# Kernel tuning notes

Measured on AMD Instinct MI355X. Metric: run time of the kernel, lower is better.

## Reference

```python
import jax, jax.numpy as jnp
import numpy as np

B, C, M, T = 2, 512, 16, 128
H = 8
D = C // H  # 64, divisible by 4 for 2D RoPE
G = C // 4  # GroupNorm groups = 128
S = M * T


def group_norm(x, scale, bias, groups=G, eps=1e-5):
    b, c, m, t = x.shape
    xg = x.reshape(b, groups, c // groups, m, t)
    mu = xg.mean(axis=(2, 3, 4), keepdims=True)
    var = xg.var(axis=(2, 3, 4), keepdims=True)
    xn = ((xg - mu) * jax.lax.rsqrt(var + eps)).reshape(b, c, m, t)
    return xn * scale[None, :, None, None] + bias[None, :, None, None]


def dwsep_conv(x, dw, pw):
    # depthwise 3x3 (groups=C) then pointwise 1x1
    y = jax.lax.conv_general_dilated(
        x, dw, window_strides=(1, 1), padding='SAME',
        dimension_numbers=('NCHW', 'HWIO', 'NCHW'), feature_group_count=x.shape[1])
    return jnp.einsum('bcmt,cd->bdmt', y, pw)


def rope2d(x):
    # x: [B,H,M,T,D]; first D/2 dims rotated by freq index m, last D/2 by time index t
    d = x.shape[-1]
    dh = d // 2
    q = dh // 2
    inv = 1.0 / (10000.0 ** (jnp.arange(q, dtype=jnp.float32) / q))

    def rot(v, ang):
        h = v.shape[-1] // 2
        v1, v2 = v[..., :h], v[..., h:]
        c, s = jnp.cos(ang), jnp.sin(ang)
        return jnp.concatenate([v1 * c - v2 * s, v1 * s + v2 * c], axis=-1)

    ang_f = jnp.arange(x.shape[2], dtype=jnp.float32)[:, None] * inv  # [M,q]
    ang_t = jnp.arange(x.shape[3], dtype=jnp.float32)[:, None] * inv  # [T,q]
    xf = rot(x[..., :dh], ang_f[:, None, :])  # broadcast over T
    xt = rot(x[..., dh:], ang_t)
    return jnp.concatenate([xf, xt], axis=-1)


def setup_inputs() -> dict:
    key = jax.random.key(0)
    ks = jax.random.split(key, 14)
    s = 0.02
    return {
        'x': jax.random.normal(ks[0], (B, C, M, T), jnp.float32),
        'lengths': jax.random.randint(ks[1], (B,), T // 2, T + 1),
        'gn_scale': jnp.ones((C,), jnp.float32),
        'gn_bias': jnp.zeros((C,), jnp.float32),
        'dw_q': jax.random.normal(ks[2], (3, 3, 1, C), jnp.float32) * s,
        'dw_k': jax.random.normal(ks[3], (3, 3, 1, C), jnp.float32) * s,
        'dw_v': jax.random.normal(ks[4], (3, 3, 1, C), jnp.float32) * s,
        'pw_q': jax.random.normal(ks[5], (C, C), jnp.float32) * s,
        'pw_k': jax.random.normal(ks[6], (C, C), jnp.float32) * s,
        'pw_v': jax.random.normal(ks[7], (C, C), jnp.float32) * s,
        'attn_w': jax.random.normal(ks[8], (C, C), jnp.float32) * s,
        'attn_b': jnp.zeros((C,), jnp.float32),
        'out_w': jax.random.normal(ks[9], (C, C), jnp.float32) * s,
        'out_b': jnp.zeros((C,), jnp.float32),
    }


def reference(x, lengths, gn_scale, gn_bias, dw_q, dw_k, dw_v, pw_q, pw_k, pw_v,
              attn_w, attn_b, out_w, out_b):
    residual = x
    xn = group_norm(x, gn_scale, gn_bias)

    def to_heads(y):  # [B,C,M,T] -> [B,H,M,T,D]
        return y.reshape(B, H, D, M, T).transpose(0, 1, 3, 4, 2)

    q = rope2d(to_heads(dwsep_conv(xn, dw_q, pw_q)))
    k = rope2d(to_heads(dwsep_conv(xn, dw_k, pw_k)))
    v = to_heads(dwsep_conv(xn, dw_v, pw_v))

    q = q.reshape(B, H, S, D)
    k = k.reshape(B, H, S, D)
    v = v.reshape(B, H, S, D)

    scores = jnp.einsum('bhsd,bhkd->bhsk', q, k) / np.sqrt(D).astype(np.float32)
    valid_t = jnp.arange(T)[None, :] < lengths[:, None]        # [B,T]
    valid = jnp.tile(valid_t, (1, M))                          # [B,S], token idx = m*T + t
    scores = jnp.where(valid[:, None, None, :], scores, jnp.float32(-1e9))
    attn = jax.nn.softmax(scores, axis=-1)
    o = jnp.einsum('bhsk,bhkd->bhsd', attn, v)                 # [B,H,S,D]

    o = o.transpose(0, 2, 1, 3).reshape(B, S, C)
    o = o @ attn_w + attn_b                                    # block output proj
    o = o.reshape(B, M, T, C).transpose(0, 3, 1, 2)            # [B,C,M,T]
    out = jnp.einsum('bcmt,cd->bdmt', o, out_w) + out_b[None, :, None, None]
    return residual + out
```

## Files before the change

### kernel.cpp

```cpp
#include <hip/hip_runtime.h>
#include <math.h>

#define CCH 512
#define SSQ 2048
#define MTOT 4096

typedef __bf16 bf16;
typedef __bf16 bf16x8 __attribute__((ext_vector_type(8)));
typedef __bf16 bf16x4 __attribute__((ext_vector_type(4)));
typedef float  f32x4  __attribute__((ext_vector_type(4)));

#define AS1 __attribute__((address_space(1)))
#define AS3 __attribute__((address_space(3)))
__device__ __forceinline__ void glds16(const void* g, void* l) {
    __builtin_amdgcn_global_load_lds((const AS1 void*)g, (AS3 void*)l, 16, 0, 0);
}

__global__ __launch_bounds__(256) void gnw_kernel(const float* __restrict__ x,
        float* __restrict__ mu, float* __restrict__ rstd,
        const float* __restrict__ w0, const float* __restrict__ w1,
        const float* __restrict__ w2, const float* __restrict__ w3,
        const float* __restrict__ w4, bf16* __restrict__ wT,
        const float* __restrict__ attnb, const float* __restrict__ outb,
        float* __restrict__ bcv) {
    __shared__ float smem[64*65];
    int tid = threadIdx.x;
    if (blockIdx.x < 256) {
        float* s_sum = smem;
        float* s_sq  = smem + 256;
        int bg = blockIdx.x;
        long base = (long)bg * 8192;
        float sum = 0.f, sq = 0.f;
#pragma unroll
        for (int r = 0; r < 32; ++r) {
            float v = x[base + r*256 + tid];
            sum += v; sq += v*v;
        }
        s_sum[tid] = sum; s_sq[tid] = sq;
        __syncthreads();
        for (int off = 128; off > 0; off >>= 1) {
            if (tid < off) { s_sum[tid] += s_sum[tid+off]; s_sq[tid] += s_sq[tid+off]; }
            __syncthreads();
        }
        if (tid == 0) {
            float m = s_sum[0] * (1.f/8192.f);
            float v = s_sq[0]  * (1.f/8192.f) - m*m;
            mu[bg] = m;
            rstd[bg] = rsqrtf(v + 1e-5f);
        }
    } else if (blockIdx.x < 576) {
        int bid = blockIdx.x - 256;
        int z = bid >> 6, r2 = bid & 63;
        int k0 = (r2 >> 3)*64, n0 = (r2 & 7)*64;
        const float* srcs[5] = {w0, w1, w2, w3, w4};
        const float* W = srcs[z];
        bf16* D = wT + (long)z * (CCH*CCH);
        float (*t)[65] = (float(*)[65])smem;
        int cI = tid & 63, r4 = tid >> 6;
#pragma unroll
        for (int p = 0; p < 16; ++p) {
            int kr = p*4 + r4;
            t[kr][cI] = W[(long)(k0+kr)*CCH + n0 + cI];
        }
        __syncthreads();
#pragma unroll
        for (int p = 0; p < 16; ++p) {
            int nr = p*4 + r4;
            D[(long)(n0+nr)*CCH + k0 + cI] = (bf16)t[cI][nr];
        }
    } else if (blockIdx.x < 578) {
        int n = (blockIdx.x - 576)*256 + tid;
        float a = outb[n];
#pragma unroll 16
        for (int j = 0; j < 512; ++j)
            a = fmaf(attnb[j], w4[(long)j*CCH + n], a);
        bcv[n] = a;
    } else {
        bf16* wAc = wT + (long)5*CCH*CCH;
        int base = (blockIdx.x - 578)*4096 + tid;
#pragma unroll
        for (int p = 0; p < 16; ++p)
            wAc[base + p*256] = (bf16)w3[base + p*256];
    }
}

__global__ void tn_kernel(const float* __restrict__ x, const float* __restrict__ mu,
                          const float* __restrict__ rstd, const float* __restrict__ gsc,
                          const float* __restrict__ gbs, bf16* __restrict__ xnT) {
    __shared__ float t[64][65];
    int s0 = blockIdx.x*64, c0 = blockIdx.y*64, b = blockIdx.z;
    int tid = threadIdx.x;
    int cI = tid & 63, r4 = tid >> 6;
#pragma unroll
    for (int p = 0; p < 16; ++p) {
        int cr = p*4 + r4;
        t[cr][cI] = x[((long)(b*CCH + c0 + cr))*SSQ + s0 + cI];
    }
    __syncthreads();
#pragma unroll
    for (int p = 0; p < 16; ++p) {
        int sr = p*4 + r4;
        int c = c0 + cI;
        int g = b*128 + (c >> 2);
        float v = (t[cI][sr] - mu[g]) * rstd[g] * gsc[c] + gbs[c];
        xnT[((long)(b*SSQ + s0 + sr))*CCH + c] = (bf16)v;
    }
}

__global__ __launch_bounds__(256) void dw3_kernel(const bf16* __restrict__ xnT,
        const float* __restrict__ dwq, const float* __restrict__ dwk,
        const float* __restrict__ dwv,
        bf16* __restrict__ yq, bf16* __restrict__ yk, bf16* __restrict__ yv) {
    int tid = threadIdx.x;
    int cc = (tid & 63) * 8;
    int s  = blockIdx.x*4 + (tid >> 6);
    int sl = s & (SSQ-1);
    int b  = s >> 11;
    int m = sl >> 7, t = sl & 127;
    float aq[8] = {}, ak[8] = {}, av[8] = {};
#pragma unroll
    for (int di = 0; di < 3; ++di) {
        int m2 = m + di - 1;
        if ((unsigned)m2 >= 16u) continue;
#pragma unroll
        for (int dj = 0; dj < 3; ++dj) {
            int t2 = t + dj - 1;
            if ((unsigned)t2 >= 128u) continue;
            bf16x8 xv = *(const bf16x8*)(xnT + ((long)(b*SSQ + m2*128 + t2))*CCH + cc);
            int wi = (di*3 + dj)*CCH + cc;
#pragma unroll
            for (int i = 0; i < 8; ++i) {
                float xf = (float)xv[i];
                aq[i] += xf * dwq[wi+i];
                ak[i] += xf * dwk[wi+i];
                av[i] += xf * dwv[wi+i];
            }
        }
    }
    bf16x8 oq, ok, ov;
#pragma unroll
    for (int i = 0; i < 8; ++i) { oq[i] = (bf16)aq[i]; ok[i] = (bf16)ak[i]; ov[i] = (bf16)av[i]; }
    long o = (long)s*CCH + cc;
    *(bf16x8*)(yq + o) = oq;
    *(bf16x8*)(yk + o) = ok;
    *(bf16x8*)(yv + o) = ov;
}

template<int NFR>
__device__ __forceinline__ void gemm_core128(const bf16* __restrict__ A,
        const bf16* __restrict__ Wt, int m0, int n0,
        bf16* As, bf16* Bs, f32x4 (&acc)[4][NFR]) {
    int tid = threadIdx.x, lane = tid & 63, wid = tid >> 6;
    int sw = wid & 1, nw = wid >> 1;
    int col = lane & 15, quad = lane >> 4;
    const char* gA[4]; char* ldsA[4];
#pragma unroll
    for (int p = 0; p < 4; ++p) {
        int ci = tid + p*256;
        int row = ci >> 3;
        int c = (ci & 7) ^ (row & 7);
        gA[p] = (const char*)A + ((long)(m0+row)*CCH + c*8)*2;
        ldsA[p] = (char*)As + ci*16;
    }
    const char* gB[NFR]; char* ldsB[NFR];
#pragma unroll
    for (int p = 0; p < NFR; ++p) {
        int ci = tid + p*256;
        int row = ci >> 3;
        int c = (ci & 7) ^ (row & 7);
        gB[p] = (const char*)Wt + ((long)(n0+row)*CCH + c*8)*2;
        ldsB[p] = (char*)Bs + ci*16;
    }
    int rowA = sw*64 + col;
    int rowB = nw*(NFR*16) + col;
    for (int k0 = 0; k0 < CCH; k0 += 64) {
        __syncthreads();
#pragma unroll
        for (int p = 0; p < 4; ++p)   glds16(gA[p] + k0*2, ldsA[p]);
#pragma unroll
        for (int p = 0; p < NFR; ++p) glds16(gB[p] + k0*2, ldsB[p]);
        __syncthreads();
        bf16x8 af[4][2], bfr[NFR][2];
#pragma unroll
        for (int mt = 0; mt < 4; ++mt) {
            int r = rowA + mt*16;
#pragma unroll
            for (int ks = 0; ks < 2; ++ks) {
                int c = (ks*4 + quad) ^ (r & 7);
                af[mt][ks] = *(const bf16x8*)((char*)As + r*128 + c*16);
            }
        }
#pragma unroll
        for (int nt = 0; nt < NFR; ++nt) {
            int r = rowB + nt*16;
#pragma unroll
            for (int ks = 0; ks < 2; ++ks) {
                int c = (ks*4 + quad) ^ (r & 7);
                bfr[nt][ks] = *(const bf16x8*)((char*)Bs + r*128 + c*16);
            }
        }
#pragma unroll
        for (int ks = 0; ks < 2; ++ks)
#pragma unroll
            for (int mt = 0; mt < 4; ++mt)
#pragma unroll
                for (int nt = 0; nt < NFR; ++nt)
                    acc[mt][nt] = __builtin_amdgcn_mfma_f32_16x16x32_bf16(
                        af[mt][ks], bfr[nt][ks], acc[mt][nt], 0,0,0);
    }
}

__global__ __launch_bounds__(256) void gemm_qkv(const bf16* __restrict__ Abase,
        bf16* __restrict__ wT, bf16* __restrict__ qout,
        bf16* __restrict__ kout, bf16* __restrict__ vout) {
    __shared__ bf16 As[128*64];
    __shared__ bf16 Bs[64*64];
    int z = blockIdx.z;
    if (z == 3 && blockIdx.x >= 4) return;
    int m0 = blockIdx.x*128, n0 = blockIdx.y*64;
    const bf16* Aop = (z < 3) ? Abase + (long)z*MTOT*CCH : wT + (long)4*CCH*CCH;
    const bf16* Wop = (z < 3) ? wT + (long)z*CCH*CCH   : wT + (long)5*CCH*CCH;
    f32x4 acc[4][2] = {};
    gemm_core128<2>(Aop, Wop, m0, n0, As, Bs, acc);
    int tid = threadIdx.x, lane = tid & 63, wid = tid >> 6;
    int sw = wid & 1, nw = wid >> 1;
    int col = lane & 15, quad = lane >> 4;
    int nb = n0 + nw*32, mb = m0 + sw*64;
    if (z == 3) {
        bf16* wCt = wT + (long)6*CCH*CCH;
#pragma unroll
        for (int nt = 0; nt < 2; ++nt) {
            int n = nb + nt*16 + col;
#pragma unroll
            for (int mt = 0; mt < 4; ++mt)
#pragma unroll
                for (int r = 0; r < 4; ++r)
                    wCt[(long)(mb + mt*16 + quad*4 + r)*CCH + n] = (bf16)acc[mt][nt][r];
        }
    } else if (z < 2) {
        bf16* outp = z ? kout : qout;
        const float sc = z ? 1.0f : 0.125f;
        float invf = __expf(-(float)col * 0.5756462732485114f);
        bool tHalf = (nb & 32) != 0;
#pragma unroll
        for (int mt = 0; mt < 4; ++mt)
#pragma unroll
            for (int r = 0; r < 4; ++r) {
                int row = mb + mt*16 + quad*4 + r;
                int sl = row & (SSQ-1);
                float pos = tHalf ? (float)(sl & 127) : (float)(sl >> 7);
                float ang = pos * invf;
                float sn, cs;
                __sincosf(ang, &sn, &cs);
                float x1 = acc[mt][0][r], x2 = acc[mt][1][r];
                outp[(long)row*CCH + nb + col]      = (bf16)((x1*cs - x2*sn)*sc);
                outp[(long)row*CCH + nb + 16 + col] = (bf16)((x1*sn + x2*cs)*sc);
            }
    } else {
#pragma unroll
        for (int mt = 0; mt < 4; ++mt)
#pragma unroll
            for (int nt = 0; nt < 2; ++nt) {
                int n = nb + nt*16 + col;
                int row0 = mb + mt*16 + quad*4;
                int bq = row0 >> 11, sl0 = row0 & (SSQ-1);
                bf16x4 pk;
#pragma unroll
                for (int r = 0; r < 4; ++r) pk[r] = (bf16)acc[mt][nt][r];
                *(bf16x4*)(vout + ((long)(bq*CCH + n))*SSQ + sl0) = pk;
            }
    }
}

__global__ __launch_bounds__(256) void gemm_out(const bf16* __restrict__ A,
        const bf16* __restrict__ Wt, const float* __restrict__ bias,
        const float* __restrict__ resid, float* __restrict__ outp) {
    __shared__ bf16 As[128*64];
    __shared__ bf16 Bs[64*64];
    int m0 = blockIdx.x*128, n0 = blockIdx.y*64;
    f32x4 acc[4][2] = {};
    gemm_core128<2>(A, Wt, m0, n0, As, Bs, acc);
    int tid = threadIdx.x, lane = tid & 63, wid = tid >> 6;
    int sw = wid & 1, nw = wid >> 1;
    int col = lane & 15, quad = lane >> 4;
    int nb = n0 + nw*32, mb = m0 + sw*64;
#pragma unroll
    for (int mt = 0; mt < 4; ++mt)
#pragma unroll
        for (int nt = 0; nt < 2; ++nt) {
            int n = nb + nt*16 + col;
            float bv = bias[n];
            int row0 = mb + mt*16 + quad*4;
            int b = row0 >> 11, sl0 = row0 & (SSQ-1);
            long off = ((long)(b*CCH + n))*SSQ + sl0;
            float4 rr = *(const float4*)(resid + off);
            float4 o4;
            o4.x = acc[mt][nt][0] + bv + rr.x;
            o4.y = acc[mt][nt][1] + bv + rr.y;
            o4.z = acc[mt][nt][2] + bv + rr.z;
            o4.w = acc[mt][nt][3] + bv + rr.w;
            *(float4*)(outp + off) = o4;
        }
}

__global__ __launch_bounds__(512, 4) void attn_kernel(
        const bf16* __restrict__ qb, const bf16* __restrict__ kb,
        const bf16* __restrict__ vb, const int* __restrict__ lengths,
        bf16* __restrict__ o) {
    __shared__ char KVs[2][32768];
    __shared__ float Lm[4][2][16];
    int bid = blockIdx.x;
    int bh = bid & 15, qtb = bid >> 4;
    int b = bh >> 3, h = bh & 7;
    int tid = threadIdx.x, wid = tid >> 6, lane = tid & 63;
    int col = lane & 15, quad = lane >> 4;
    int qh = wid & 3, kh = wid >> 2;
    int q0 = qtb*128 + qh*32;
    int thr = lengths[b] - 64 - quad*4;

    const char* gp[4]; int ldsoff[4];
#pragma unroll
    for (int p = 0; p < 4; ++p) {
        int idx = tid + p*512;
        int half = p >> 1;
        int rem = idx & 511;
        int r = rem >> 3;
        int csrc = (rem & 7) ^ (r & 7);
        if ((p & 1) == 0)
            gp[p] = (const char*)kb + ((long)(b*SSQ + half*1024 + r))*1024 + h*128 + csrc*16;
        else
            gp[p] = (const char*)vb + ((long)(b*CCH + h*64 + r))*4096 + half*2048 + csrc*16;
        ldsoff[p] = idx*16;
    }

    const bf16* qp = qb + (long)(b*SSQ)*CCH + h*64;
    bf16x8 qf[2][2];
#pragma unroll
    for (int qt2 = 0; qt2 < 2; ++qt2)
#pragma unroll
        for (int dc = 0; dc < 2; ++dc)
            qf[qt2][dc] = *(const bf16x8*)(qp + (long)(q0 + qt2*16 + col)*CCH + dc*32 + quad*8);

    f32x4 of[2][4] = {};
    float ls0 = 0.f, ls1 = 0.f;
    int cswz = col & 7;
    int kbase0 = col*128 + ((0*4 + quad) ^ cswz)*16;
    int kbase1 = col*128 + ((1*4 + quad) ^ cswz)*16;
    int qh2 = quad >> 1, qlo = (quad & 1)*8;
    int vlo0 = col*128 + ((0 + qh2) ^ cswz)*16 + qlo;
    int vhi0 = col*128 + ((4 + qh2) ^ cswz)*16 + qlo;
    int vlo1 = col*128 + ((2 + qh2) ^ cswz)*16 + qlo;
    int vhi1 = col*128 + ((6 + qh2) ^ cswz)*16 + qlo;

#pragma unroll
    for (int p = 0; p < 4; ++p) glds16(gp[p], KVs[0] + ldsoff[p]);
    __syncthreads();

    for (int t = 0; t < 16; ++t) {
        if (t < 15) {
#pragma unroll
            for (int p = 0; p < 4; ++p) {
                long step = (p & 1) ? 128L : 65536L;
                glds16(gp[p] + (long)(t+1)*step, KVs[(t+1) & 1] + ldsoff[p]);
            }
        }
        const char* K = KVs[t & 1] + kh*16384;
        const char* V = K + 8192;
        f32x4 sc[4][2];
        if (t & 1) {
#pragma unroll
            for (int sub = 0; sub < 4; ++sub) {
                f32x4 m;
#pragma unroll
                for (int r = 0; r < 4; ++r) m[r] = (sub*16 + r < thr) ? 0.f : -10000.f;
                sc[sub][0] = m; sc[sub][1] = m;
            }
        } else {
#pragma unroll
            for (int sub = 0; sub < 4; ++sub) {
                sc[sub][0] = (f32x4){0.f,0.f,0.f,0.f};
                sc[sub][1] = (f32x4){0.f,0.f,0.f,0.f};
            }
        }
        __builtin_amdgcn_s_setprio(1);
#pragma unroll
        for (int sub = 0; sub < 4; ++sub) {
            bf16x8 kf0 = *(const bf16x8*)(K + sub*2048 + kbase0);
            bf16x8 kf1 = *(const bf16x8*)(K + sub*2048 + kbase1);
            sc[sub][0] = __builtin_amdgcn_mfma_f32_16x16x32_bf16(kf0, qf[0][0], sc[sub][0], 0,0,0);
            sc[sub][1] = __builtin_amdgcn_mfma_f32_16x16x32_bf16(kf0, qf[1][0], sc[sub][1], 0,0,0);
            sc[sub][0] = __builtin_amdgcn_mfma_f32_16x16x32_bf16(kf1, qf[0][1], sc[sub][0], 0,0,0);
            sc[sub][1] = __builtin_amdgcn_mfma_f32_16x16x32_bf16(kf1, qf[1][1], sc[sub][1], 0,0,0);
        }
        __builtin_amdgcn_s_setprio(0);
#pragma unroll
        for (int ks = 0; ks < 2; ++ks) {
            bf16x8 pf[2];
#pragma unroll
            for (int qt2 = 0; qt2 < 2; ++qt2) {
                float s = 0.f;
#pragma unroll
                for (int r = 0; r < 4; ++r) {
                    float e0 = __expf(sc[ks][qt2][r]);
                    float e1 = __expf(sc[ks+2][qt2][r]);
                    pf[qt2][r]     = (bf16)e0;
                    pf[qt2][4 + r] = (bf16)e1;
                    s += e0 + e1;
                }
                if (qt2) ls1 += s; else ls0 += s;
            }
            int vlo = ks ? vlo1 : vlo0;
            int vhi = ks ? vhi1 : vhi0;
            __builtin_amdgcn_s_setprio(1);
#pragma unroll
            for (int dt = 0; dt < 4; ++dt) {
                bf16x4 lo = *(const bf16x4*)(V + dt*2048 + vlo);
                bf16x4 hi = *(const bf16x4*)(V + dt*2048 + vhi);
                bf16x8 vf = {lo[0],lo[1],lo[2],lo[3],hi[0],hi[1],hi[2],hi[3]};
                of[0][dt] = __builtin_amdgcn_mfma_f32_16x16x32_bf16(pf[0], vf, of[0][dt], 0,0,0);
                of[1][dt] = __builtin_amdgcn_mfma_f32_16x16x32_bf16(pf[1], vf, of[1][dt], 0,0,0);
            }
            __builtin_amdgcn_s_setprio(0);
        }
        __syncthreads();
    }

    ls0 += __shfl_xor(ls0, 16); ls0 += __shfl_xor(ls0, 32);
    ls1 += __shfl_xor(ls1, 16); ls1 += __shfl_xor(ls1, 32);

    float* Om = (float*)KVs;
    if (kh == 1) {
#pragma unroll
        for (int qt2 = 0; qt2 < 2; ++qt2)
#pragma unroll
            for (int dt = 0; dt < 4; ++dt)
#pragma unroll
                for (int r = 0; r < 4; ++r)
                    Om[(qh*32 + qt2*16 + quad*4 + r)*64 + dt*16 + col] = of[qt2][dt][r];
        if (quad == 0) { Lm[qh][0][col] = ls0; Lm[qh][1][col] = ls1; }
    }
    __syncthreads();
    if (kh == 0) {
        float i0 = 1.f / (ls0 + Lm[qh][0][col]);
        float i1 = 1.f / (ls1 + Lm[qh][1][col]);
        bf16* ob = o + (long)(b*SSQ + q0)*CCH + h*64;
#pragma unroll
        for (int qt2 = 0; qt2 < 2; ++qt2) {
            float inv = qt2 ? i1 : i0;
            float ir[4];
#pragma unroll
            for (int r = 0; r < 4; ++r) ir[r] = __shfl(inv, quad*4 + r);
#pragma unroll
            for (int dt = 0; dt < 4; ++dt)
#pragma unroll
                for (int r = 0; r < 4; ++r) {
                    float v = of[qt2][dt][r] + Om[(qh*32 + qt2*16 + quad*4 + r)*64 + dt*16 + col];
                    ob[(long)(qt2*16 + quad*4 + r)*CCH + dt*16 + col] = (bf16)(v * ir[r]);
                }
        }
    }
}

extern "C" void kernel_launch(void* const* d_in, const int* in_sizes, int n_in,
                              void* d_out, int out_size, void* d_ws, size_t ws_size,
                              hipStream_t stream) {
    const float* x        = (const float*)d_in[0];
    const int*   lengths  = (const int*)  d_in[1];
    const float* gn_scale = (const float*)d_in[2];
    const float* gn_bias  = (const float*)d_in[3];
    const float* dw_q     = (const float*)d_in[4];
    const float* dw_k     = (const float*)d_in[5];
    const float* dw_v     = (const float*)d_in[6];
    const float* pw_q     = (const float*)d_in[7];
    const float* pw_k     = (const float*)d_in[8];
    const float* pw_v     = (const float*)d_in[9];
    const float* attn_w   = (const float*)d_in[10];
    const float* attn_b   = (const float*)d_in[11];
    const float* out_w    = (const float*)d_in[12];
    const float* out_b    = (const float*)d_in[13];
    float* out = (float*)d_out;

    char* w = (char*)d_ws;
    float* mu   = (float*)w;
    float* rstd = (float*)(w + 1024);
    float* bcv  = (float*)(w + 2048);
    bf16* wT    = (bf16*)(w + 4096);
    bf16* wCt = wT + (long)6*CCH*CCH;
    bf16* xnT  = (bf16*)(w + 0x00400000);
    bf16* yT   = (bf16*)(w + 0x00800000);
    bf16* qbf  = (bf16*)(w + 0x01400000);
    bf16* kbf  = (bf16*)(w + 0x01800000);
    bf16* vbf  = (bf16*)(w + 0x01C00000);
    bf16* obf  = (bf16*)(w + 0x02000000);

    gnw_kernel<<<642, 256, 0, stream>>>(x, mu, rstd, pw_q, pw_k, pw_v, attn_w, out_w,
                                        wT, attn_b, out_b, bcv);
    tn_kernel<<<dim3(32,8,2), 256, 0, stream>>>(x, mu, rstd, gn_scale, gn_bias, xnT);
    dw3_kernel<<<MTOT/4, 256, 0, stream>>>(xnT, dw_q, dw_k, dw_v,
                                           yT, yT + (long)MTOT*CCH, yT + (long)2*MTOT*CCH);

    gemm_qkv<<<dim3(MTOT/128, CCH/64, 4), 256, 0, stream>>>(yT, wT, qbf, kbf, vbf);

    attn_kernel<<<256, 512, 0, stream>>>(qbf, kbf, vbf, lengths, obf);

    gemm_out<<<dim3(MTOT/128, CCH/64), 256, 0, stream>>>(obf, wCt, bcv, x, out);
}
```

Before: 176.9 us.

## Restructure attention to split keys across waves with 64-query blocks

The attention kernel now uses 256-thread blocks over 64 queries each (512 blocks). Each of the four waves handles a 32-key slice of every 128-key tile for all 64 queries, and the four partial outputs are reduced through LDS at the end. The V producer in the QKV GEMM writes a permuted sequence order so each lane can read V fragments with a single 16-byte LDS load instead of two 8-byte loads. The aim is more K/V fragment reuse across query tiles and fewer LDS reads, at the cost of a larger cross-wave reduction, more registers per wave and lower occupancy.

```diff
diff --git a/kernel.cpp b/kernel.cpp
--- a/kernel.cpp
+++ b/kernel.cpp
@@ -264,10 +264,12 @@
                 int n = nb + nt*16 + col;
                 int row0 = mb + mt*16 + quad*4;
                 int bq = row0 >> 11, sl0 = row0 & (SSQ-1);
+                int sub16 = (sl0 >> 4) & 1;
+                long slp = (long)(sl0 & ~31) + quad*8 + sub16*4;
                 bf16x4 pk;
 #pragma unroll
                 for (int r = 0; r < 4; ++r) pk[r] = (bf16)acc[mt][nt][r];
-                *(bf16x4*)(vout + ((long)(bq*CCH + n))*SSQ + sl0) = pk;
+                *(bf16x4*)(vout + ((long)(bq*CCH + n))*SSQ + slp) = pk;
             }
     }
 }
@@ -303,161 +305,139 @@
         }
 }
 
-__global__ __launch_bounds__(512, 4) void attn_kernel(
+__global__ __launch_bounds__(256, 2) void attn_kernel(
         const bf16* __restrict__ qb, const bf16* __restrict__ kb,
         const bf16* __restrict__ vb, const int* __restrict__ lengths,
         bf16* __restrict__ o) {
     __shared__ char KVs[2][32768];
-    __shared__ float Lm[4][2][16];
+    __shared__ float Lsm[4][4][16];
     int bid = blockIdx.x;
     int bh = bid & 15, qtb = bid >> 4;
     int b = bh >> 3, h = bh & 7;
     int tid = threadIdx.x, wid = tid >> 6, lane = tid & 63;
     int col = lane & 15, quad = lane >> 4;
-    int qh = wid & 3, kh = wid >> 2;
-    int q0 = qtb*128 + qh*32;
-    int thr = lengths[b] - 64 - quad*4;
-
-    const char* gp[4]; int ldsoff[4];
-#pragma unroll
-    for (int p = 0; p < 4; ++p) {
-        int idx = tid + p*512;
-        int half = p >> 1;
-        int rem = idx & 511;
-        int r = rem >> 3;
-        int csrc = (rem & 7) ^ (r & 7);
-        if ((p & 1) == 0)
-            gp[p] = (const char*)kb + ((long)(b*SSQ + half*1024 + r))*1024 + h*128 + csrc*16;
-        else
-            gp[p] = (const char*)vb + ((long)(b*CCH + h*64 + r))*4096 + half*2048 + csrc*16;
+    int q0 = qtb*64;
+    int lenb = lengths[b];
+    int thr = lenb - wid*32 - quad*4;
+
+    const char* gp[8]; int ldsoff[8];
+#pragma unroll
+    for (int p = 0; p < 8; ++p) {
+        int idx = p*256 + tid;
+        if (p < 4) {
+            int r = idx >> 3;
+            int csrc = (idx & 7) ^ (r & 7);
+            gp[p] = (const char*)kb + ((long)(b*SSQ + r))*1024 + h*128 + csrc*16;
+        } else {
+            int rem = idx & 1023;
+            int r = rem >> 4;
+            int csrc = (rem & 15) ^ (r & 15);
+            gp[p] = (const char*)vb + ((long)(b*CCH + h*64 + r))*4096 + csrc*16;
+        }
         ldsoff[p] = idx*16;
     }
 
     const bf16* qp = qb + (long)(b*SSQ)*CCH + h*64;
-    bf16x8 qf[2][2];
-#pragma unroll
-    for (int qt2 = 0; qt2 < 2; ++qt2)
+    bf16x8 qf[4][2];
+#pragma unroll
+    for (int qt = 0; qt < 4; ++qt)
 #pragma unroll
         for (int dc = 0; dc < 2; ++dc)
-            qf[qt2][dc] = *(const bf16x8*)(qp + (long)(q0 + qt2*16 + col)*CCH + dc*32 + quad*8);
-
-    f32x4 of[2][4] = {};
-    float ls0 = 0.f, ls1 = 0.f;
-    int cswz = col & 7;
-    int kbase0 = col*128 + ((0*4 + quad) ^ cswz)*16;
-    int kbase1 = col*128 + ((1*4 + quad) ^ cswz)*16;
-    int qh2 = quad >> 1, qlo = (quad & 1)*8;
-    int vlo0 = col*128 + ((0 + qh2) ^ cswz)*16 + qlo;
-    int vhi0 = col*128 + ((4 + qh2) ^ cswz)*16 + qlo;
-    int vlo1 = col*128 + ((2 + qh2) ^ cswz)*16 + qlo;
-    int vhi1 = col*128 + ((6 + qh2) ^ cswz)*16 + qlo;
-
-#pragma unroll
-    for (int p = 0; p < 4; ++p) glds16(gp[p], KVs[0] + ldsoff[p]);
+            qf[qt][dc] = *(const bf16x8*)(qp + (long)(q0 + qt*16 + col)*CCH + dc*32 + quad*8);
+
+    f32x4 of[4][4] = {};
+    float ls[4] = {};
+    int cswz7 = col & 7;
+    int kc0 = (quad ^ cswz7)*16;
+    int kc1 = ((4 + quad) ^ cswz7)*16;
+    int vaddr = col*256 + (((wid*4 + quad) ^ col) & 15)*16;
+
+#pragma unroll
+    for (int p = 0; p < 8; ++p) glds16(gp[p], KVs[0] + ldsoff[p]);
     __syncthreads();
 
     for (int t = 0; t < 16; ++t) {
         if (t < 15) {
 #pragma unroll
-            for (int p = 0; p < 4; ++p) {
-                long step = (p & 1) ? 128L : 65536L;
+            for (int p = 0; p < 8; ++p) {
+                const long step = (p < 4) ? 131072L : 256L;
                 glds16(gp[p] + (long)(t+1)*step, KVs[(t+1) & 1] + ldsoff[p]);
             }
         }
-        const char* K = KVs[t & 1] + kh*16384;
-        const char* V = K + 8192;
-        f32x4 sc[4][2];
-        if (t & 1) {
-#pragma unroll
-            for (int sub = 0; sub < 4; ++sub) {
-                f32x4 m;
-#pragma unroll
-                for (int r = 0; r < 4; ++r) m[r] = (sub*16 + r < thr) ? 0.f : -10000.f;
-                sc[sub][0] = m; sc[sub][1] = m;
-            }
-        } else {
-#pragma unroll
-            for (int sub = 0; sub < 4; ++sub) {
-                sc[sub][0] = (f32x4){0.f,0.f,0.f,0.f};
-                sc[sub][1] = (f32x4){0.f,0.f,0.f,0.f};
-            }
+        const char* K = KVs[t & 1] + wid*4096;
+        const char* V = KVs[t & 1] + 16384;
+        f32x4 sc[2][4];
+#pragma unroll
+        for (int sub = 0; sub < 2; ++sub) {
+            f32x4 m;
+#pragma unroll
+            for (int r = 0; r < 4; ++r) m[r] = (sub*16 + r < thr) ? 0.f : -10000.f;
+#pragma unroll
+            for (int qt = 0; qt < 4; ++qt) sc[sub][qt] = m;
         }
         __builtin_amdgcn_s_setprio(1);
 #pragma unroll
-        for (int sub = 0; sub < 4; ++sub) {
-            bf16x8 kf0 = *(const bf16x8*)(K + sub*2048 + kbase0);
-            bf16x8 kf1 = *(const bf16x8*)(K + sub*2048 + kbase1);
-            sc[sub][0] = __builtin_amdgcn_mfma_f32_16x16x32_bf16(kf0, qf[0][0], sc[sub][0], 0,0,0);
-            sc[sub][1] = __builtin_amdgcn_mfma_f32_16x16x32_bf16(kf0, qf[1][0], sc[sub][1], 0,0,0);
-            sc[sub][0] = __builtin_amdgcn_mfma_f32_16x16x32_bf16(kf1, qf[0][1], sc[sub][0], 0,0,0);
-            sc[sub][1] = __builtin_amdgcn_mfma_f32_16x16x32_bf16(kf1, qf[1][1], sc[sub][1], 0,0,0);
+        for (int sub = 0; sub < 2; ++sub) {
+            bf16x8 kf0 = *(const bf16x8*)(K + sub*2048 + col*128 + kc0);
+            bf16x8 kf1 = *(const bf16x8*)(K + sub*2048 + col*128 + kc1);
+#pragma unroll
+            for (int qt = 0; qt < 4; ++qt) {
+                sc[sub][qt] = __builtin_amdgcn_mfma_f32_16x16x32_bf16(kf0, qf[qt][0], sc[sub][qt], 0,0,0);
+                sc[sub][qt] = __builtin_amdgcn_mfma_f32_16x16x32_bf16(kf1, qf[qt][1], sc[sub][qt], 0,0,0);
+            }
         }
         __builtin_amdgcn_s_setprio(0);
-#pragma unroll
-        for (int ks = 0; ks < 2; ++ks) {
-            bf16x8 pf[2];
-#pragma unroll
-            for (int qt2 = 0; qt2 < 2; ++qt2) {
-                float s = 0.f;
-#pragma unroll
-                for (int r = 0; r < 4; ++r) {
-                    float e0 = __expf(sc[ks][qt2][r]);
-                    float e1 = __expf(sc[ks+2][qt2][r]);
-                    pf[qt2][r]     = (bf16)e0;
-                    pf[qt2][4 + r] = (bf16)e1;
-                    s += e0 + e1;
-                }
-                if (qt2) ls1 += s; else ls0 += s;
-            }
-            int vlo = ks ? vlo1 : vlo0;
-            int vhi = ks ? vhi1 : vhi0;
-            __builtin_amdgcn_s_setprio(1);
-#pragma unroll
-            for (int dt = 0; dt < 4; ++dt) {
-                bf16x4 lo = *(const bf16x4*)(V + dt*2048 + vlo);
-                bf16x4 hi = *(const bf16x4*)(V + dt*2048 + vhi);
-                bf16x8 vf = {lo[0],lo[1],lo[2],lo[3],hi[0],hi[1],hi[2],hi[3]};
-                of[0][dt] = __builtin_amdgcn_mfma_f32_16x16x32_bf16(pf[0], vf, of[0][dt], 0,0,0);
-                of[1][dt] = __builtin_amdgcn_mfma_f32_16x16x32_bf16(pf[1], vf, of[1][dt], 0,0,0);
-            }
-            __builtin_amdgcn_s_setprio(0);
-        }
+        bf16x8 pf[4];
+#pragma unroll
+        for (int qt = 0; qt < 4; ++qt) {
+            float s = 0.f;
+#pragma unroll
+            for (int r = 0; r < 4; ++r) {
+                float e0 = __expf(sc[0][qt][r]);
+                float e1 = __expf(sc[1][qt][r]);
+                pf[qt][r]     = (bf16)e0;
+                pf[qt][4 + r] = (bf16)e1;
+                s += e0 + e1;
+            }
+            ls[qt] += s;
+        }
+        __builtin_amdgcn_s_setprio(1);
+#pragma unroll
+        for (int dt = 0; dt < 4; ++dt) {
+            bf16x8 vf = *(const bf16x8*)(V + dt*4096 + vaddr);
+#pragma unroll
+            for (int qt = 0; qt < 4; ++qt)
+                of[qt][dt] = __builtin_amdgcn_mfma_f32_16x16x32_bf16(pf[qt], vf, of[qt][dt], 0,0,0);
+        }
+        __builtin_amdgcn_s_setprio(0);
         __syncthreads();
     }
 
-    ls0 += __shfl_xor(ls0, 16); ls0 += __shfl_xor(ls0, 32);
-    ls1 += __shfl_xor(ls1, 16); ls1 += __shfl_xor(ls1, 32);
-
+#pragma unroll
+    for (int qt = 0; qt < 4; ++qt) {
+        ls[qt] += __shfl_xor(ls[qt], 16);
+        ls[qt] += __shfl_xor(ls[qt], 32);
+    }
     float* Om = (float*)KVs;
-    if (kh == 1) {
-#pragma unroll
-        for (int qt2 = 0; qt2 < 2; ++qt2)
-#pragma unroll
-            for (int dt = 0; dt < 4; ++dt)
-#pragma unroll
-                for (int r = 0; r < 4; ++r)
-                    Om[(qh*32 + qt2*16 + quad*4 + r)*64 + dt*16 + col] = of[qt2][dt][r];
-        if (quad == 0) { Lm[qh][0][col] = ls0; Lm[qh][1][col] = ls1; }
-    }
+#pragma unroll
+    for (int qt = 0; qt < 4; ++qt)
+#pragma unroll
+        for (int dt = 0; dt < 4; ++dt)
+#pragma unroll
+            for (int r = 0; r < 4; ++r)
+                Om[(wid*64 + qt*16 + quad*4 + r)*64 + dt*16 + col] = of[qt][dt][r];
+    if (quad == 0)
+#pragma unroll
+        for (int qt = 0; qt < 4; ++qt) Lsm[wid][qt][col] = ls[qt];
     __syncthreads();
-    if (kh == 0) {
-        float i0 = 1.f / (ls0 + Lm[qh][0][col]);
-        float i1 = 1.f / (ls1 + Lm[qh][1][col]);
-        bf16* ob = o + (long)(b*SSQ + q0)*CCH + h*64;
-#pragma unroll
-        for (int qt2 = 0; qt2 < 2; ++qt2) {
-            float inv = qt2 ? i1 : i0;
-            float ir[4];
-#pragma unroll
-            for (int r = 0; r < 4; ++r) ir[r] = __shfl(inv, quad*4 + r);
-#pragma unroll
-            for (int dt = 0; dt < 4; ++dt)
-#pragma unroll
-                for (int r = 0; r < 4; ++r) {
-                    float v = of[qt2][dt][r] + Om[(qh*32 + qt2*16 + quad*4 + r)*64 + dt*16 + col];
-                    ob[(long)(qt2*16 + quad*4 + r)*CCH + dt*16 + col] = (bf16)(v * ir[r]);
-                }
-        }
+    bf16* ob = o + (long)(b*SSQ + q0)*CCH + h*64;
+#pragma unroll
+    for (int i = 0; i < 16; ++i) {
+        int rr = wid*16 + i;
+        float v = Om[rr*64 + lane] + Om[(64 + rr)*64 + lane]
+                + Om[(128 + rr)*64 + lane] + Om[(192 + rr)*64 + lane];
+        float l = Lsm[0][wid][i] + Lsm[1][wid][i] + Lsm[2][wid][i] + Lsm[3][wid][i];
+        ob[(long)rr*CCH + lane] = (bf16)(v / l);
     }
 }
 
@@ -501,7 +481,7 @@
 
     gemm_qkv<<<dim3(MTOT/128, CCH/64, 4), 256, 0, stream>>>(yT, wT, qbf, kbf, vbf);
 
-    attn_kernel<<<256, 512, 0, stream>>>(qbf, kbf, vbf, lengths, obf);
+    attn_kernel<<<512, 256, 0, stream>>>(qbf, kbf, vbf, lengths, obf);
 
     gemm_out<<<dim3(MTOT/128, CCH/64), 256, 0, stream>>>(obf, wCt, bcv, x, out);
 }
```

Result: faster. 163.8 us (-7.4%).
